# Optimization experiments

Measured on AMD Instinct MI355X. Metric: run time of the kernel, lower is better.

## Reference

```python
import jax, jax.numpy as jnp
import numpy as np

B, T, C, D, P = 8, 512, 32, 128, 1024
EPS = 1e-5

def setup_inputs() -> dict:
    key = jax.random.key(0)
    ks = jax.random.split(key, 11)
    s = 1.0 / np.sqrt(D)
    inp = {
        'x': jax.random.normal(ks[0], (B, T, C, D), jnp.float32),
        'x_mask': jax.random.randint(ks[1], (B, T, C), 0, 2) == 1,
        'p_mask': jax.random.randint(ks[2], (B, T, C), 0, 2) == 1,
        'pos': jax.random.randint(ks[3], (B, T, C), 0, P),
        'pe': jax.random.normal(ks[4], (P, D // 2, 2), jnp.float32),  # complex rpe as [re, im]
        'imp': jax.random.randint(ks[5], (B, T), 0, C),
        'idx_c': jax.random.randint(ks[6], (B, T, C), 0, C),
        'wq_w': jax.random.normal(ks[7], (D, D), jnp.float32) * s,
        'wq_b': jnp.zeros((D,), jnp.float32),
        'wk_w': jax.random.normal(ks[8], (D, D), jnp.float32) * s,
        'wk_b': jnp.zeros((D,), jnp.float32),
        'wv_w': jax.random.normal(ks[9], (D, D), jnp.float32) * s,
        'wv_b': jnp.zeros((D,), jnp.float32),
        'ls_gamma': 1e-5 * jnp.ones((D,), jnp.float32),
        'ln_gamma': jnp.ones((D,), jnp.float32),
        'ln_beta': jnp.zeros((D,), jnp.float32),
    }
    return inp


def _rotate(z, r):
    # z: (b,t,c,d) real; r: (b,t,c,d/2,2) complex multiplier [re,im]
    b, t, c, d = z.shape
    zr = z.reshape(b, t, c, d // 2, 2)
    re = zr[..., 0] * r[..., 0] - zr[..., 1] * r[..., 1]
    im = zr[..., 0] * r[..., 1] + zr[..., 1] * r[..., 0]
    return jnp.stack([re, im], axis=-1).reshape(b, t, c, d)


def reference(x, x_mask, p_mask, pos, pe, imp, idx_c,
              wq_w, wq_b, wk_w, wk_b, wv_w, wv_b,
              ls_gamma, ln_gamma, ln_beta):
    b, t, c, d = x.shape
    # channel selection gather: where x_mask, use per-token important channel
    imp_rep = jnp.broadcast_to(imp[:, :, None], (b, t, c))
    idx = jnp.where(x_mask, imp_rep, idx_c)            # (b,t,c)
    xg = jnp.take_along_axis(x, idx[..., None], axis=2)  # (b,t,c,d)
    # QKV projections (torch Linear: x @ W.T + b)
    q = xg @ wq_w.T + wq_b
    k = xg @ wk_w.T + wk_b
    v = xg @ wv_w.T + wv_b
    # relative PE complex rotation on q,k
    r = pe[pos]                                        # (b,t,c,d/2,2)
    q = _rotate(q, r)
    k = _rotate(k, r)
    # (b,c,t,d) layout; channel acts as head
    qt = q.transpose(0, 2, 1, 3)
    kt = k.transpose(0, 2, 1, 3)
    vt = v.transpose(0, 2, 1, 3)
    scores = jnp.einsum('bcqd,bckd->bcqk', qt, kt) / jnp.sqrt(jnp.float32(d))
    pm = p_mask.transpose(0, 2, 1)                     # (b,c,t)
    mask = pm[:, :, :, None] | pm[:, :, None, :]       # (b,c,t,t)
    attn = jax.nn.softmax(jnp.where(mask, -jnp.inf, scores), axis=-1)
    attn = jnp.nan_to_num(attn)
    xm = x_mask.transpose(0, 2, 1)                     # (b,c,t)
    weight = jnp.where(xm, 1.0 / t, 1.0)
    out = jnp.einsum('bcmn,bcnd->bmcd', attn * weight[:, :, None, :], vt)  # (b,t,c,d)
    # norm_first=False: LN(x + layer_scale(out))
    y = x + ls_gamma * out
    mu = jnp.mean(y, axis=-1, keepdims=True)
    var = jnp.mean(jnp.square(y - mu), axis=-1, keepdims=True)
    return (y - mu) / jnp.sqrt(var + EPS) * ln_gamma + ln_beta
```

## Files before the change

kernel.cpp:

```cpp
#include <hip/hip_runtime.h>
#include <hip/hip_bf16.h>

#define Bb 8
#define Tt 512
#define Cc 32
#define Dd 128
#define SCALE 0.08838834764831845f
#define SROW 520

typedef unsigned int u32;
typedef __hip_bfloat16 bf16;
typedef __attribute__((ext_vector_type(8))) short short8;
typedef __attribute__((ext_vector_type(4))) short short4v;
typedef __attribute__((ext_vector_type(4))) float floatx4;

__device__ __forceinline__ short f2bf(float f) {
    __hip_bfloat16 h = __float2bfloat16(f);
    return *(short*)&h;
}
__device__ __forceinline__ float bf2f(short s) {
    return __uint_as_float(((u32)(unsigned short)s) << 16);
}

__global__ __launch_bounds__(256)
void k_wconv(const float* __restrict__ wq, const float* __restrict__ wk,
             const float* __restrict__ wv, short* __restrict__ Wb)
{
    int g = blockIdx.x * 256 + threadIdx.x;
    int mat = g >> 14, rem = g & 16383;
    const float* src = (mat == 0) ? wq : (mat == 1) ? wk : wv;
    Wb[g] = f2bf(src[rem]);
}

__global__ __launch_bounds__(256)
void k_qkvm(const float* __restrict__ x, const int* __restrict__ xm,
            const int* __restrict__ pos, const float* __restrict__ pe,
            const int* __restrict__ imp, const int* __restrict__ idxc,
            const short* __restrict__ Wb,
            const float* __restrict__ bq, const float* __restrict__ bk,
            const float* __restrict__ bv,
            short* __restrict__ qb, short* __restrict__ kb, short* __restrict__ vb)
{
    const int R0  = blockIdx.x * 64;
    const int b   = R0 >> 14;
    const int t0  = (R0 >> 5) & 511;
    const int tid = threadIdx.x;
    const int w    = tid >> 6;
    const int lane = tid & 63;
    const int quad = lane >> 4;
    const int m    = lane & 15;

    __shared__ short xg[64 * 136];
    __shared__ short ot[64 * 392];

#pragma unroll
    for (int i = 0; i < 8; ++i) {
        int u   = tid + i * 256;
        int row = u >> 5, seg = u & 31;
        int R   = R0 + row;
        int idx = xm[R] ? imp[R >> 5] : idxc[R];
        float4 v = *(const float4*)(x + ((long)(R >> 5) * Cc + idx) * Dd + seg * 4);
        short4v s = {f2bf(v.x), f2bf(v.y), f2bf(v.z), f2bf(v.w)};
        *(short4v*)&xg[row * 136 + seg * 4] = s;
    }

    short8 wf[6][4];
    float  bias_v[6];
#pragma unroll
    for (int mat = 0; mat < 3; ++mat) {
        const float* bp = (mat == 0) ? bq : (mat == 1) ? bk : bv;
#pragma unroll
        for (int h = 0; h < 2; ++h) {
            int sl = mat * 2 + h;
            int ct = h * 4 + w;
            bias_v[sl] = bp[ct * 16 + m];
#pragma unroll
            for (int kb = 0; kb < 4; ++kb)
                wf[sl][kb] = *(const short8*)(Wb + ((long)mat * 128 + ct * 16 + m) * 128
                                              + kb * 32 + quad * 8);
        }
    }
    __syncthreads();

    for (int rt = 0; rt < 4; ++rt) {
        short8 af[4];
#pragma unroll
        for (int kb = 0; kb < 4; ++kb)
            af[kb] = *(const short8*)&xg[(rt * 16 + m) * 136 + kb * 32 + quad * 8];

        floatx4 acc[6];
#pragma unroll
        for (int sl = 0; sl < 6; ++sl) acc[sl] = (floatx4){0.f, 0.f, 0.f, 0.f};
#pragma unroll
        for (int kb = 0; kb < 4; ++kb)
#pragma unroll
            for (int sl = 0; sl < 6; ++sl)
                acc[sl] = __builtin_amdgcn_mfma_f32_16x16x32_bf16(af[kb], wf[sl][kb], acc[sl], 0, 0, 0);

        int po[4];
#pragma unroll
        for (int r = 0; r < 4; ++r) po[r] = pos[R0 + rt * 16 + quad * 4 + r];

#pragma unroll
        for (int sl = 0; sl < 6; ++sl) {
            int mat = sl >> 1;
            int ct  = (sl & 1) * 4 + w;
            int d   = ct * 16 + m;
#pragma unroll
            for (int r = 0; r < 4; ++r) {
                float v = acc[sl][r] + bias_v[sl];
                float p = __shfl_xor(v, 1, 64);
                if (mat < 2) {
                    const float* rp = pe + ((long)po[r] * (Dd / 2) + (d >> 1)) * 2;
                    float r0 = rp[0], r1 = rp[1];
                    v = (d & 1) ? fmaf(p, r1, v * r0) : fmaf(v, r0, -(p * r1));
                    if (mat == 0) v *= SCALE;
                }
                ot[(rt * 16 + quad * 4 + r) * 392 + mat * 128 + d] = f2bf(v);
            }
        }
    }
    __syncthreads();

    short* const mats[3] = {qb, kb, vb};
#pragma unroll
    for (int mat = 0; mat < 3; ++mat) {
        short* dst = mats[mat];
#pragma unroll
        for (int i = 0; i < 4; ++i) {
            int g = tid + i * 256;
            int n = g >> 4, off = (g & 15) * 8;
            int c = n & 31, tl = n >> 5;
            *(short8*)(dst + (((long)(b * Cc + c) * Tt) + t0 + tl) * Dd + off) =
                *(const short8*)&ot[n * 392 + mat * 128 + off];
        }
    }
}

__global__ __launch_bounds__(256)
void k_vt(const short* __restrict__ vb, const int* __restrict__ xm,
          short* __restrict__ vt)
{
    const int head = blockIdx.y;
    const int b    = head >> 5;
    const int c    = head & 31;
    const int t0   = blockIdx.x * 64;
    const int tid  = threadIdx.x;

    __shared__ short tile[64 * 136];
    __shared__ float wks[64];

    if (tid < 64)
        wks[tid] = xm[((long)b * Tt + t0 + tid) * Cc + c] ? (1.0f / Tt) : 1.0f;

    const short* src = vb + ((long)head * Tt + t0) * Dd;
#pragma unroll
    for (int i = 0; i < 4; ++i) {
        int u = tid + i * 256;
        int row = u >> 4, col = (u & 15) * 8;
        *(short8*)&tile[row * 136 + col] = *(const short8*)(src + row * Dd + col);
    }
    __syncthreads();

    short* dst = vt + (long)head * Dd * Tt + t0;
#pragma unroll
    for (int i = 0; i < 4; ++i) {
        int u = tid + i * 256;
        int d = u >> 3, t8 = (u & 7) * 8;
        short8 v;
#pragma unroll
        for (int j = 0; j < 8; ++j)
            v[j] = f2bf(bf2f(tile[(t8 + j) * 136 + d]) * wks[t8 + j]);
        *(short8*)(dst + (long)d * Tt + t8) = v;
    }
}

__global__ __launch_bounds__(256, 4)
void k_attn(const short* __restrict__ qb, const short* __restrict__ kbp,
            const short* __restrict__ vtp, const float* __restrict__ x,
            const int* __restrict__ pm,
            const float* __restrict__ lsg, const float* __restrict__ lng,
            const float* __restrict__ lnb, float* __restrict__ out)
{
    const int head = blockIdx.y;
    const int b    = head >> 5;
    const int c    = head & 31;
    const int qt0  = blockIdx.x * 32;
    const int tid  = threadIdx.x;
    const int w    = tid >> 6;
    const int lane = tid & 63;
    const int quad = lane >> 4;
    const int m    = lane & 15;

    __shared__ short S[32 * SROW];
    __shared__ u32   pkbits[16];
    __shared__ float rlS[32];
    __shared__ float ps1[4][32];
    __shared__ float ps2[4][32];
    __shared__ float mrs[32][2];

#pragma unroll
    for (int p = 0; p < 2; ++p) {
        int i = p * 256 + tid;
        bool v = pm[((long)b * Tt + i) * Cc + c] != 0;
        unsigned long long bal = __ballot(v);
        if (lane == 0) {
            pkbits[p * 8 + w * 2]     = (u32)bal;
            pkbits[p * 8 + w * 2 + 1] = (u32)(bal >> 32);
        }
    }

    short8 qf[2][4];
#pragma unroll
    for (int qt = 0; qt < 2; ++qt)
#pragma unroll
        for (int kb = 0; kb < 4; ++kb)
            qf[qt][kb] = *(const short8*)(qb + ((long)head * Tt + qt0 + qt * 16 + m) * Dd
                                          + kb * 32 + quad * 8);
    __syncthreads();

#pragma unroll 2
    for (int ch = 0; ch < 8; ++ch) {
        const short* kp = kbp + ((long)head * Tt + ch * 64 + w * 16 + m) * Dd + quad * 8;
        floatx4 sc0 = {0.f, 0.f, 0.f, 0.f}, sc1 = {0.f, 0.f, 0.f, 0.f};
#pragma unroll
        for (int kb = 0; kb < 4; ++kb) {
            short8 bk = *(const short8*)(kp + kb * 32);
            sc0 = __builtin_amdgcn_mfma_f32_16x16x32_bf16(qf[0][kb], bk, sc0, 0, 0, 0);
            sc1 = __builtin_amdgcn_mfma_f32_16x16x32_bf16(qf[1][kb], bk, sc1, 0, 0, 0);
        }
        int kt = ch * 64 + w * 16 + m;
        u32 wbits = pkbits[ch * 2 + ((w * 16 + m) >> 5)];
        bool masked = (wbits >> ((w * 16 + m) & 31)) & 1;
#pragma unroll
        for (int r = 0; r < 4; ++r) {
            S[(quad * 4 + r) * SROW + kt]      = f2bf(masked ? -1e30f : sc0[r]);
            S[(16 + quad * 4 + r) * SROW + kt] = f2bf(masked ? -1e30f : sc1[r]);
        }
    }
    __syncthreads();

    {
        int qi = tid >> 3, part = tid & 7;
        float mx = -1e30f;
        for (int j = 0; j < 64; ++j) mx = fmaxf(mx, bf2f(S[qi * SROW + j * 8 + part]));
        mx = fmaxf(mx, __shfl_xor(mx, 1, 64));
        mx = fmaxf(mx, __shfl_xor(mx, 2, 64));
        mx = fmaxf(mx, __shfl_xor(mx, 4, 64));
        float l = 0.f;
        for (int j = 0; j < 64; ++j) {
            int kt = j * 8 + part;
            float s = bf2f(S[qi * SROW + kt]);
            float e = (s <= -1e29f) ? 0.f : __expf(s - mx);
            S[qi * SROW + kt] = f2bf(e);
            l += e;
        }
        l += __shfl_xor(l, 1, 64);
        l += __shfl_xor(l, 2, 64);
        l += __shfl_xor(l, 4, 64);
        if (part == 0) {
            bool qmask = (pkbits[blockIdx.x] >> qi) & 1;
            rlS[qi] = (l > 0.f && !qmask) ? 1.0f / l : 0.f;
        }
    }
    __syncthreads();

    floatx4 oa[2][2];
#pragma unroll
    for (int qt = 0; qt < 2; ++qt)
#pragma unroll
        for (int dt = 0; dt < 2; ++dt) oa[qt][dt] = (floatx4){0.f, 0.f, 0.f, 0.f};

    const short* vbase = vtp + (long)head * Dd * Tt;
#pragma unroll 2
    for (int ch = 0; ch < 8; ++ch) {
#pragma unroll
        for (int kb = 0; kb < 2; ++kb) {
            int tcol = ch * 64 + kb * 32 + quad * 8;
            short8 bv0 = *(const short8*)(vbase + ((long)((w * 2 + 0) * 16 + m)) * Tt + tcol);
            short8 bv1 = *(const short8*)(vbase + ((long)((w * 2 + 1) * 16 + m)) * Tt + tcol);
#pragma unroll
            for (int qt = 0; qt < 2; ++qt) {
                short8 ap = *(const short8*)&S[(qt * 16 + m) * SROW + tcol];
                oa[qt][0] = __builtin_amdgcn_mfma_f32_16x16x32_bf16(ap, bv0, oa[qt][0], 0, 0, 0);
                oa[qt][1] = __builtin_amdgcn_mfma_f32_16x16x32_bf16(ap, bv1, oa[qt][1], 0, 0, 0);
            }
        }
    }

    float yv[2][2][4];
    float s1[2][4], s2[2][4];
#pragma unroll
    for (int qt = 0; qt < 2; ++qt)
#pragma unroll
        for (int r = 0; r < 4; ++r) { s1[qt][r] = 0.f; s2[qt][r] = 0.f; }

#pragma unroll
    for (int qt = 0; qt < 2; ++qt)
#pragma unroll
        for (int dt = 0; dt < 2; ++dt) {
            int d = (w * 2 + dt) * 16 + m;
            float lg = lsg[d];
#pragma unroll
            for (int r = 0; r < 4; ++r) {
                int row = qt * 16 + quad * 4 + r;
                int t = qt0 + row;
                float val = oa[qt][dt][r] * rlS[row];
                float y = x[(((long)b * Tt + t) * Cc + c) * Dd + d] + lg * val;
                yv[qt][dt][r] = y;
                s1[qt][r] += y;
                s2[qt][r] += y * y;
            }
        }
#pragma unroll
    for (int qt = 0; qt < 2; ++qt)
#pragma unroll
        for (int r = 0; r < 4; ++r) {
            float a = s1[qt][r], bb = s2[qt][r];
            a += __shfl_xor(a, 1, 64); bb += __shfl_xor(bb, 1, 64);
            a += __shfl_xor(a, 2, 64); bb += __shfl_xor(bb, 2, 64);
            a += __shfl_xor(a, 4, 64); bb += __shfl_xor(bb, 4, 64);
            a += __shfl_xor(a, 8, 64); bb += __shfl_xor(bb, 8, 64);
            if (m == 0) {
                ps1[w][qt * 16 + quad * 4 + r] = a;
                ps2[w][qt * 16 + quad * 4 + r] = bb;
            }
        }
    __syncthreads();
    if (tid < 32) {
        float a = 0.f, bb = 0.f;
#pragma unroll
        for (int wv = 0; wv < 4; ++wv) { a += ps1[wv][tid]; bb += ps2[wv][tid]; }
        float mean = a * (1.0f / Dd);
        float var  = bb * (1.0f / Dd) - mean * mean;
        mrs[tid][0] = mean;
        mrs[tid][1] = rsqrtf(var + 1e-5f);
    }
    __syncthreads();

#pragma unroll
    for (int qt = 0; qt < 2; ++qt)
#pragma unroll
        for (int dt = 0; dt < 2; ++dt) {
            int d = (w * 2 + dt) * 16 + m;
            float g = lng[d], be = lnb[d];
#pragma unroll
            for (int r = 0; r < 4; ++r) {
                int row = qt * 16 + quad * 4 + r;
                int t = qt0 + row;
                out[(((long)b * Tt + t) * Cc + c) * Dd + d] =
                    (yv[qt][dt][r] - mrs[row][0]) * mrs[row][1] * g + be;
            }
        }
}

extern "C" void kernel_launch(void* const* d_in, const int* in_sizes, int n_in,
                              void* d_out, int out_size, void* d_ws, size_t ws_size,
                              hipStream_t stream) {
    const float* x    = (const float*)d_in[0];
    const int* xmask  = (const int*)d_in[1];
    const int* pmask  = (const int*)d_in[2];
    const int* pos    = (const int*)d_in[3];
    const float* pe   = (const float*)d_in[4];
    const int* imp    = (const int*)d_in[5];
    const int* idxc   = (const int*)d_in[6];
    const float* wq_w = (const float*)d_in[7];
    const float* wq_b = (const float*)d_in[8];
    const float* wk_w = (const float*)d_in[9];
    const float* wk_b = (const float*)d_in[10];
    const float* wv_w = (const float*)d_in[11];
    const float* wv_b = (const float*)d_in[12];
    const float* lsg  = (const float*)d_in[13];
    const float* lng  = (const float*)d_in[14];
    const float* lnb  = (const float*)d_in[15];
    float* out = (float*)d_out;

    size_t n = (size_t)Bb * Cc * Tt * Dd;
    short* qb = (short*)d_ws;
    short* kb = qb + n;
    short* vb = kb + n;
    short* vt = vb + n;
    short* Wb = vt + n;

    k_wconv<<<dim3(3 * Dd * Dd / 256), dim3(256), 0, stream>>>(wq_w, wk_w, wv_w, Wb);
    k_qkvm<<<dim3(Bb * Tt * Cc / 64), dim3(256), 0, stream>>>(
        x, xmask, pos, pe, imp, idxc, Wb, wq_b, wk_b, wv_b, qb, kb, vb);
    k_vt<<<dim3(Tt / 64, Bb * Cc), dim3(256), 0, stream>>>(vb, xmask, vt);
    k_attn<<<dim3(Tt / 32, Bb * Cc), dim3(256), 0, stream>>>(
        qb, kb, vt, x, pmask, lsg, lng, lnb, out);
}
```

Before: 351.8 us.

## Enlarge attention tile to 64 queries per 512-thread block with vectorized softmax

The attention kernel now handles 64 query rows per block with 8 waves instead of 32 rows with 4 waves, so each loaded K and V fragment feeds four MFMA query tiles. This halves redundant K/V reads from global memory. The grid is transposed so blocks of the same head are adjacent, and the softmax pass reads and writes its contiguous row slice as short8 vectors instead of scalar strided LDS accesses. Shared memory per block doubles to about 66KB and register use rises, which may reduce occupancy.

```diff
diff --git a/kernel.cpp b/kernel.cpp
--- a/kernel.cpp
+++ b/kernel.cpp
@@ -175,145 +175,139 @@
     }
 }
 
-__global__ __launch_bounds__(256, 4)
+__global__ __launch_bounds__(512, 4)
 void k_attn(const short* __restrict__ qb, const short* __restrict__ kbp,
             const short* __restrict__ vtp, const float* __restrict__ x,
             const int* __restrict__ pm,
             const float* __restrict__ lsg, const float* __restrict__ lng,
             const float* __restrict__ lnb, float* __restrict__ out)
 {
-    const int head = blockIdx.y;
+    const int head = blockIdx.x;
     const int b    = head >> 5;
     const int c    = head & 31;
-    const int qt0  = blockIdx.x * 32;
+    const int qt0  = blockIdx.y * 64;
     const int tid  = threadIdx.x;
     const int w    = tid >> 6;
     const int lane = tid & 63;
     const int quad = lane >> 4;
     const int m    = lane & 15;
 
-    __shared__ short S[32 * SROW];
+    __shared__ short S[64 * SROW];
     __shared__ u32   pkbits[16];
-    __shared__ float rlS[32];
-    __shared__ float ps1[4][32];
-    __shared__ float ps2[4][32];
-    __shared__ float mrs[32][2];
-
-#pragma unroll
-    for (int p = 0; p < 2; ++p) {
-        int i = p * 256 + tid;
-        bool v = pm[((long)b * Tt + i) * Cc + c] != 0;
+    __shared__ float rlS[64];
+    __shared__ float ps1[8][64];
+    __shared__ float ps2[8][64];
+    __shared__ float mrs[64][2];
+
+    {
+        bool v = pm[((long)b * Tt + tid) * Cc + c] != 0;
         unsigned long long bal = __ballot(v);
         if (lane == 0) {
-            pkbits[p * 8 + w * 2]     = (u32)bal;
-            pkbits[p * 8 + w * 2 + 1] = (u32)(bal >> 32);
-        }
-    }
-
-    short8 qf[2][4];
-#pragma unroll
-    for (int qt = 0; qt < 2; ++qt)
+            pkbits[w * 2]     = (u32)bal;
+            pkbits[w * 2 + 1] = (u32)(bal >> 32);
+        }
+    }
+
+    short8 qf[4][4];
+#pragma unroll
+    for (int qt = 0; qt < 4; ++qt)
 #pragma unroll
         for (int kb = 0; kb < 4; ++kb)
             qf[qt][kb] = *(const short8*)(qb + ((long)head * Tt + qt0 + qt * 16 + m) * Dd
                                           + kb * 32 + quad * 8);
     __syncthreads();
 
-#pragma unroll 2
-    for (int ch = 0; ch < 8; ++ch) {
-        const short* kp = kbp + ((long)head * Tt + ch * 64 + w * 16 + m) * Dd + quad * 8;
-        floatx4 sc0 = {0.f, 0.f, 0.f, 0.f}, sc1 = {0.f, 0.f, 0.f, 0.f};
+    for (int ch = 0; ch < 4; ++ch) {
+        int kt = ch * 128 + w * 16 + m;
+        const short* kp = kbp + ((long)head * Tt + kt) * Dd + quad * 8;
+        floatx4 sc[4];
+#pragma unroll
+        for (int qt = 0; qt < 4; ++qt) sc[qt] = (floatx4){0.f, 0.f, 0.f, 0.f};
 #pragma unroll
         for (int kb = 0; kb < 4; ++kb) {
             short8 bk = *(const short8*)(kp + kb * 32);
-            sc0 = __builtin_amdgcn_mfma_f32_16x16x32_bf16(qf[0][kb], bk, sc0, 0, 0, 0);
-            sc1 = __builtin_amdgcn_mfma_f32_16x16x32_bf16(qf[1][kb], bk, sc1, 0, 0, 0);
-        }
-        int kt = ch * 64 + w * 16 + m;
-        u32 wbits = pkbits[ch * 2 + ((w * 16 + m) >> 5)];
-        bool masked = (wbits >> ((w * 16 + m) & 31)) & 1;
-#pragma unroll
-        for (int r = 0; r < 4; ++r) {
-            S[(quad * 4 + r) * SROW + kt]      = f2bf(masked ? -1e30f : sc0[r]);
-            S[(16 + quad * 4 + r) * SROW + kt] = f2bf(masked ? -1e30f : sc1[r]);
-        }
+#pragma unroll
+            for (int qt = 0; qt < 4; ++qt)
+                sc[qt] = __builtin_amdgcn_mfma_f32_16x16x32_bf16(qf[qt][kb], bk, sc[qt], 0, 0, 0);
+        }
+        bool masked = (pkbits[kt >> 5] >> (kt & 31)) & 1;
+#pragma unroll
+        for (int qt = 0; qt < 4; ++qt)
+#pragma unroll
+            for (int r = 0; r < 4; ++r)
+                S[(qt * 16 + quad * 4 + r) * SROW + kt] = f2bf(masked ? -1e30f : sc[qt][r]);
     }
     __syncthreads();
 
     {
         int qi = tid >> 3, part = tid & 7;
+        short* rowp = &S[qi * SROW + part * 64];
+        short8 sv[8];
+#pragma unroll
+        for (int j = 0; j < 8; ++j) sv[j] = *(short8*)&rowp[j * 8];
         float mx = -1e30f;
-        for (int j = 0; j < 64; ++j) mx = fmaxf(mx, bf2f(S[qi * SROW + j * 8 + part]));
+#pragma unroll
+        for (int j = 0; j < 8; ++j)
+#pragma unroll
+            for (int e = 0; e < 8; ++e) mx = fmaxf(mx, bf2f(sv[j][e]));
         mx = fmaxf(mx, __shfl_xor(mx, 1, 64));
         mx = fmaxf(mx, __shfl_xor(mx, 2, 64));
         mx = fmaxf(mx, __shfl_xor(mx, 4, 64));
         float l = 0.f;
-        for (int j = 0; j < 64; ++j) {
-            int kt = j * 8 + part;
-            float s = bf2f(S[qi * SROW + kt]);
-            float e = (s <= -1e29f) ? 0.f : __expf(s - mx);
-            S[qi * SROW + kt] = f2bf(e);
-            l += e;
-        }
+#pragma unroll
+        for (int j = 0; j < 8; ++j)
+#pragma unroll
+            for (int e = 0; e < 8; ++e) {
+                float s = bf2f(sv[j][e]);
+                float ex = (s <= -1e29f) ? 0.f : __expf(s - mx);
+                sv[j][e] = f2bf(ex);
+                l += ex;
+            }
+#pragma unroll
+        for (int j = 0; j < 8; ++j) *(short8*)&rowp[j * 8] = sv[j];
         l += __shfl_xor(l, 1, 64);
         l += __shfl_xor(l, 2, 64);
         l += __shfl_xor(l, 4, 64);
         if (part == 0) {
-            bool qmask = (pkbits[blockIdx.x] >> qi) & 1;
+            int t = qt0 + qi;
+            bool qmask = (pkbits[t >> 5] >> (t & 31)) & 1;
             rlS[qi] = (l > 0.f && !qmask) ? 1.0f / l : 0.f;
         }
     }
     __syncthreads();
 
-    floatx4 oa[2][2];
-#pragma unroll
-    for (int qt = 0; qt < 2; ++qt)
-#pragma unroll
-        for (int dt = 0; dt < 2; ++dt) oa[qt][dt] = (floatx4){0.f, 0.f, 0.f, 0.f};
-
-    const short* vbase = vtp + (long)head * Dd * Tt;
-#pragma unroll 2
-    for (int ch = 0; ch < 8; ++ch) {
-#pragma unroll
-        for (int kb = 0; kb < 2; ++kb) {
-            int tcol = ch * 64 + kb * 32 + quad * 8;
-            short8 bv0 = *(const short8*)(vbase + ((long)((w * 2 + 0) * 16 + m)) * Tt + tcol);
-            short8 bv1 = *(const short8*)(vbase + ((long)((w * 2 + 1) * 16 + m)) * Tt + tcol);
-#pragma unroll
-            for (int qt = 0; qt < 2; ++qt) {
-                short8 ap = *(const short8*)&S[(qt * 16 + m) * SROW + tcol];
-                oa[qt][0] = __builtin_amdgcn_mfma_f32_16x16x32_bf16(ap, bv0, oa[qt][0], 0, 0, 0);
-                oa[qt][1] = __builtin_amdgcn_mfma_f32_16x16x32_bf16(ap, bv1, oa[qt][1], 0, 0, 0);
-            }
-        }
-    }
-
-    float yv[2][2][4];
-    float s1[2][4], s2[2][4];
-#pragma unroll
-    for (int qt = 0; qt < 2; ++qt)
-#pragma unroll
-        for (int r = 0; r < 4; ++r) { s1[qt][r] = 0.f; s2[qt][r] = 0.f; }
-
-#pragma unroll
-    for (int qt = 0; qt < 2; ++qt)
-#pragma unroll
-        for (int dt = 0; dt < 2; ++dt) {
-            int d = (w * 2 + dt) * 16 + m;
-            float lg = lsg[d];
-#pragma unroll
-            for (int r = 0; r < 4; ++r) {
-                int row = qt * 16 + quad * 4 + r;
-                int t = qt0 + row;
-                float val = oa[qt][dt][r] * rlS[row];
-                float y = x[(((long)b * Tt + t) * Cc + c) * Dd + d] + lg * val;
-                yv[qt][dt][r] = y;
-                s1[qt][r] += y;
-                s2[qt][r] += y * y;
-            }
-        }
-#pragma unroll
-    for (int qt = 0; qt < 2; ++qt)
+    floatx4 oa[4];
+#pragma unroll
+    for (int qt = 0; qt < 4; ++qt) oa[qt] = (floatx4){0.f, 0.f, 0.f, 0.f};
+
+    const short* vbase = vtp + (long)head * Dd * Tt + ((long)(w * 16 + m)) * Tt + quad * 8;
+    for (int kv = 0; kv < 16; ++kv) {
+        short8 bv = *(const short8*)(vbase + kv * 32);
+#pragma unroll
+        for (int qt = 0; qt < 4; ++qt) {
+            short8 ap = *(const short8*)&S[(qt * 16 + m) * SROW + kv * 32 + quad * 8];
+            oa[qt] = __builtin_amdgcn_mfma_f32_16x16x32_bf16(ap, bv, oa[qt], 0, 0, 0);
+        }
+    }
+
+    const int d = w * 16 + m;
+    const float lg = lsg[d];
+    float yv[4][4];
+    float s1[4][4], s2[4][4];
+#pragma unroll
+    for (int qt = 0; qt < 4; ++qt)
+#pragma unroll
+        for (int r = 0; r < 4; ++r) {
+            int row = qt * 16 + quad * 4 + r;
+            int t = qt0 + row;
+            float val = oa[qt][r] * rlS[row];
+            float y = x[(((long)b * Tt + t) * Cc + c) * Dd + d] + lg * val;
+            yv[qt][r] = y;
+            s1[qt][r] = y;
+            s2[qt][r] = y * y;
+        }
+#pragma unroll
+    for (int qt = 0; qt < 4; ++qt)
 #pragma unroll
         for (int r = 0; r < 4; ++r) {
             float a = s1[qt][r], bb = s2[qt][r];
@@ -327,10 +321,10 @@
             }
         }
     __syncthreads();
-    if (tid < 32) {
+    if (tid < 64) {
         float a = 0.f, bb = 0.f;
 #pragma unroll
-        for (int wv = 0; wv < 4; ++wv) { a += ps1[wv][tid]; bb += ps2[wv][tid]; }
+        for (int wv = 0; wv < 8; ++wv) { a += ps1[wv][tid]; bb += ps2[wv][tid]; }
         float mean = a * (1.0f / Dd);
         float var  = bb * (1.0f / Dd) - mean * mean;
         mrs[tid][0] = mean;
@@ -338,19 +332,15 @@
     }
     __syncthreads();
 
-#pragma unroll
-    for (int qt = 0; qt < 2; ++qt)
-#pragma unroll
-        for (int dt = 0; dt < 2; ++dt) {
-            int d = (w * 2 + dt) * 16 + m;
-            float g = lng[d], be = lnb[d];
-#pragma unroll
-            for (int r = 0; r < 4; ++r) {
-                int row = qt * 16 + quad * 4 + r;
-                int t = qt0 + row;
-                out[(((long)b * Tt + t) * Cc + c) * Dd + d] =
-                    (yv[qt][dt][r] - mrs[row][0]) * mrs[row][1] * g + be;
-            }
+    const float g = lng[d], be = lnb[d];
+#pragma unroll
+    for (int qt = 0; qt < 4; ++qt)
+#pragma unroll
+        for (int r = 0; r < 4; ++r) {
+            int row = qt * 16 + quad * 4 + r;
+            int t = qt0 + row;
+            out[(((long)b * Tt + t) * Cc + c) * Dd + d] =
+                (yv[qt][r] - mrs[row][0]) * mrs[row][1] * g + be;
         }
 }
 
@@ -386,6 +376,6 @@
     k_qkvm<<<dim3(Bb * Tt * Cc / 64), dim3(256), 0, stream>>>(
         x, xmask, pos, pe, imp, idxc, Wb, wq_b, wk_b, wv_b, qb, kb, vb);
     k_vt<<<dim3(Tt / 64, Bb * Cc), dim3(256), 0, stream>>>(vb, xmask, vt);
-    k_attn<<<dim3(Tt / 32, Bb * Cc), dim3(256), 0, stream>>>(
+    k_attn<<<dim3(Bb * Cc, Tt / 64), dim3(512), 0, stream>>>(
         qb, kb, vt, x, pmask, lsg, lng, lnb, out);
 }
```

New measurement: 327.5 us. 6.9% less time.
